# Kernel tuning notes

Hardware: AMD Instinct MI355X
Metric: run time of the kernel (lower is better)

## Reference

```python
import jax, jax.numpy as jnp
import numpy as np

EMBED_DIM = 768
D_K = 64
B, S = 4, 4096


def setup_inputs() -> dict:
    key = jax.random.key(0)
    ks = jax.random.split(key, 7)
    scale = 1.0 / np.sqrt(EMBED_DIM)
    return {
        "x": jax.random.normal(ks[0], (B, S, EMBED_DIM), dtype=jnp.float32),
        "Wq": jax.random.normal(ks[1], (EMBED_DIM, D_K), dtype=jnp.float32) * scale,
        "bq": jax.random.normal(ks[2], (D_K,), dtype=jnp.float32) * 0.01,
        "Wk": jax.random.normal(ks[3], (EMBED_DIM, D_K), dtype=jnp.float32) * scale,
        "bk": jax.random.normal(ks[4], (D_K,), dtype=jnp.float32) * 0.01,
        "Wv": jax.random.normal(ks[5], (EMBED_DIM, D_K), dtype=jnp.float32) * scale,
        "bv": jax.random.normal(ks[6], (D_K,), dtype=jnp.float32) * 0.01,
    }


def reference(x, Wq, bq, Wk, bk, Wv, bv):
    # Linear projections: [B, S, E] @ [E, d_k] + bias -> [B, S, d_k]
    q = jnp.einsum("bse,ed->bsd", x, Wq) + bq
    k = jnp.einsum("bse,ed->bsd", x, Wk) + bk
    v = jnp.einsum("bse,ed->bsd", x, Wv) + bv
    # Scaled dot-product attention; scores: [B, S, S]
    scores = jnp.einsum("bqd,bkd->bqk", q, k) / jnp.sqrt(jnp.asarray(D_K, x.dtype))
    attn = jax.nn.softmax(scores, axis=-1)
    return jnp.einsum("bqk,bkd->bqd", attn, v)
```

## Files before the change

kernel.cpp:

```cpp
#include <hip/hip_runtime.h>

typedef _Float16 f16;
typedef f16 f16x2 __attribute__((ext_vector_type(2)));
typedef f16 f16x4 __attribute__((ext_vector_type(4)));
typedef f16 f16x8 __attribute__((ext_vector_type(8)));
typedef float f32x4 __attribute__((ext_vector_type(4)));

#define MFMA32(A, B, C) __builtin_amdgcn_mfma_f32_16x16x32_f16(A, B, C, 0, 0, 0)
#define MFMA16(A, B, C) __builtin_amdgcn_mfma_f32_16x16x16f16(A, B, C, 0, 0, 0)

#define QSCALE (0.125f * 1.44269504088896340736f)
#define MSHIFT 10.0f

__device__ __forceinline__ f16x2 pkrtz(float a, float b) {
  return __builtin_bit_cast(f16x2, __builtin_amdgcn_cvt_pkrtz(a, b));
}
__device__ __forceinline__ void nts(f16* p, f16x8 v) {
  __builtin_nontemporal_store(v, (f16x8*)p);
}
__device__ __forceinline__ f16x8 ntl(const f16* p) {
  return __builtin_nontemporal_load((const f16x8*)p);
}

__global__ __launch_bounds__(256) void wtrans_kernel(
    const float* __restrict__ Wq, const float* __restrict__ Wk,
    const float* __restrict__ Wv, f16* __restrict__ Wt) {
  __shared__ float T[64][65];
  const int t = threadIdx.x;
  const int kt = blockIdx.x;
  const int z = blockIdx.y;
  const float* W = (z == 0) ? Wq : ((z == 1) ? Wk : Wv);

  {
    const int kl = t >> 2, c0 = (t & 3) * 16;
    const float* wp = W + (kt * 64 + kl) * 64 + c0;
    float4 v0 = *(const float4*)wp;
    float4 v1 = *(const float4*)(wp + 4);
    float4 v2 = *(const float4*)(wp + 8);
    float4 v3 = *(const float4*)(wp + 12);
    float* Tr = &T[kl][c0];
    Tr[0] = v0.x; Tr[1] = v0.y; Tr[2] = v0.z; Tr[3] = v0.w;
    Tr[4] = v1.x; Tr[5] = v1.y; Tr[6] = v1.z; Tr[7] = v1.w;
    Tr[8] = v2.x; Tr[9] = v2.y; Tr[10] = v2.z; Tr[11] = v2.w;
    Tr[12] = v3.x; Tr[13] = v3.y; Tr[14] = v3.z; Tr[15] = v3.w;
  }
  __syncthreads();
  {
    const int n = t >> 2, k0 = (t & 3) * 16;
    union { f16x2 h2[8]; f16x8 h8[2]; } u;
#pragma unroll
    for (int i = 0; i < 8; i++)
      u.h2[i] = pkrtz(T[k0 + 2 * i][n], T[k0 + 2 * i + 1][n]);
    f16* dst = Wt + (z * 64 + n) * 768 + kt * 64 + k0;
    *(f16x8*)dst = u.h8[0];
    *(f16x8*)(dst + 8) = u.h8[1];
  }
}

__global__ __launch_bounds__(256, 4) void proj_kernel(
    const float* __restrict__ x, const f16* __restrict__ Wt,
    const float* __restrict__ bq, const float* __restrict__ bk,
    const float* __restrict__ bv, f16* __restrict__ qo, f16* __restrict__ ko,
    f16* __restrict__ vt) {
  __shared__ f16 Xs[32][72];
  __shared__ f16 Ws[192][72];

  const int t = threadIdx.x;
  const int w = t >> 6;
  const int lane = t & 63;
  const int ln = lane & 15;
  const int quad = lane >> 4;
  const int mh = w & 1;
  const int nh = w >> 1;
  const int r0 = blockIdx.x * 32;

  f32x4 acc[6];
#pragma unroll
  for (int i = 0; i < 6; i++) acc[i] = (f32x4){0.f, 0.f, 0.f, 0.f};

  const int xsr = t >> 3, xsc = (t & 7) * 8;
  const int wsr = t >> 2, wsc = (t & 3) * 16;
  const float* xr = x + (r0 + xsr) * 768 + xsc;
  const f16* wr = Wt + wsr * 768 + wsc;

  float4 xa0, xa1;
  f16x8 wf[3][2];
  xa0 = *(const float4*)xr;
  xa1 = *(const float4*)(xr + 4);
#pragma unroll
  for (int p = 0; p < 3; p++) {
    wf[p][0] = *(const f16x8*)(wr + p * 64 * 768);
    wf[p][1] = *(const f16x8*)(wr + p * 64 * 768 + 8);
  }

  for (int kc = 0; kc < 12; kc++) {
    __syncthreads();
    {
      union { f16x2 h2[4]; f16x8 h8; } u;
      u.h2[0] = pkrtz(xa0.x, xa0.y); u.h2[1] = pkrtz(xa0.z, xa0.w);
      u.h2[2] = pkrtz(xa1.x, xa1.y); u.h2[3] = pkrtz(xa1.z, xa1.w);
      *(f16x8*)&Xs[xsr][xsc] = u.h8;
#pragma unroll
      for (int p = 0; p < 3; p++) {
        *(f16x8*)&Ws[p * 64 + wsr][wsc] = wf[p][0];
        *(f16x8*)&Ws[p * 64 + wsr][wsc + 8] = wf[p][1];
      }
    }
    if (kc + 1 < 12) {
      const float* xp = xr + (kc + 1) * 64;
      xa0 = *(const float4*)xp;
      xa1 = *(const float4*)(xp + 4);
      const f16* wp = wr + (kc + 1) * 64;
#pragma unroll
      for (int p = 0; p < 3; p++) {
        wf[p][0] = *(const f16x8*)(wp + p * 64 * 768);
        wf[p][1] = *(const f16x8*)(wp + p * 64 * 768 + 8);
      }
    }
    __syncthreads();

    f16x8 a0 = *(const f16x8*)&Xs[mh * 16 + ln][quad * 8];
    f16x8 a1 = *(const f16x8*)&Xs[mh * 16 + ln][32 + quad * 8];
#pragma unroll
    for (int nt = 0; nt < 6; nt++) {
      f16x8 b0 = *(const f16x8*)&Ws[nh * 96 + nt * 16 + ln][quad * 8];
      f16x8 b1 = *(const f16x8*)&Ws[nh * 96 + nt * 16 + ln][32 + quad * 8];
      acc[nt] = MFMA32(a0, b0, acc[nt]);
      acc[nt] = MFMA32(a1, b1, acc[nt]);
    }
  }

  const int rowg = r0 + mh * 16 + quad * 4;
  if (nh == 0) {
#pragma unroll
    for (int nt = 0; nt < 4; nt++) {
      int d = nt * 16 + ln;
      float bb = bq[d];
#pragma unroll
      for (int r = 0; r < 4; r++)
        qo[(rowg + r) * 64 + d] = (f16)((acc[nt][r] + bb) * QSCALE);
    }
#pragma unroll
    for (int nt = 4; nt < 6; nt++) {
      int d = nt * 16 + ln - 64;
      float bb = bk[d];
#pragma unroll
      for (int r = 0; r < 4; r++)
        ko[(rowg + r) * 64 + d] = (f16)(acc[nt][r] + bb);
    }
  } else {
#pragma unroll
    for (int nt = 0; nt < 2; nt++) {
      int d = 32 + nt * 16 + ln;
      float bb = bk[d];
#pragma unroll
      for (int r = 0; r < 4; r++)
        ko[(rowg + r) * 64 + d] = (f16)(acc[nt][r] + bb);
    }
    const int bidx = rowg >> 12;
    const int sb = rowg & 4095;
#pragma unroll
    for (int nt = 2; nt < 6; nt++) {
      int dv = nt * 16 + ln - 32;
      float bb = bv[dv];
      f16x4 hv;
#pragma unroll
      for (int r = 0; r < 4; r++) hv[r] = (f16)(acc[nt][r] + bb);
      *(f16x4*)&vt[((bidx * 64 + dv) << 12) + sb] = hv;
    }
  }
}

__global__ __launch_bounds__(512, 4) void attn_kernel(
    const f16* __restrict__ qo, const f16* __restrict__ ko,
    const f16* __restrict__ vt, f16* __restrict__ po, float* __restrict__ pl) {
  constexpr int CS = 8, NK = 4096 / CS;
  __shared__ f16 Ksh[64][76];
  __shared__ f16 Vsh[64][76];

  const int t = threadIdx.x;
  const int w = t >> 6;
  const int lane = t & 63;
  const int ln = lane & 15;
  const int quad = lane >> 4;
  const int bid = blockIdx.x;
  const int c = bid & 7;
  const int qb = bid >> 3;
  const int b = qb >> 4;

  f16x8 bq0[2], bq1[2];
#pragma unroll
  for (int h = 0; h < 2; h++) {
    const int qoff = (qb * 256 + w * 32 + h * 16 + ln) * 64 + quad * 8;
    bq0[h] = *(const f16x8*)(qo + qoff);
    bq1[h] = *(const f16x8*)(qo + qoff + 32);
  }

  f32x4 o[2][4];
#pragma unroll
  for (int h = 0; h < 2; h++)
#pragma unroll
    for (int i = 0; i < 4; i++) o[h][i] = (f32x4){0.f, 0.f, 0.f, 0.f};
  float l_s[2] = {0.f, 0.f};

  const int rr = t >> 3;
  const int cc = (t & 7) * 8;
  const f16* kbase = ko + (b * 4096 + c * NK) * 64;
  const f16* vbase = vt + b * 64 * 4096 + c * NK;

  f16x8 kreg = *(const f16x8*)(kbase + rr * 64 + cc);
  f16x8 vreg = *(const f16x8*)(vbase + rr * 4096 + cc);

  for (int kt = 0; kt < NK / 64; kt++) {
    __syncthreads();
    *(f16x8*)&Ksh[rr][cc] = kreg;
    *(f16x8*)&Vsh[rr][cc] = vreg;
    __syncthreads();

    if (kt + 1 < NK / 64) {
      const int ks1 = (kt + 1) * 64;
      kreg = *(const f16x8*)(kbase + (ks1 + rr) * 64 + cc);
      vreg = *(const f16x8*)(vbase + rr * 4096 + ks1 + cc);
    }

    f16x8 ka[4], kb[4];
#pragma unroll
    for (int nt = 0; nt < 4; nt++) {
      ka[nt] = *(const f16x8*)&Ksh[nt * 16 + ln][quad * 8];
      kb[nt] = *(const f16x8*)&Ksh[nt * 16 + ln][32 + quad * 8];
    }

#pragma unroll
    for (int h = 0; h < 2; h++) {
      f32x4 st[4];
#pragma unroll
      for (int i = 0; i < 4; i++) st[i] = (f32x4){0.f, 0.f, 0.f, 0.f};
#pragma unroll
      for (int nt = 0; nt < 4; nt++) {
        st[nt] = MFMA32(ka[nt], bq0[h], st[nt]);
        st[nt] = MFMA32(kb[nt], bq1[h], st[nt]);
      }

      f16x4 pa[4];
#pragma unroll
      for (int nt = 0; nt < 4; nt++) {
        float p0 = exp2f(st[nt][0] - MSHIFT);
        float p1 = exp2f(st[nt][1] - MSHIFT);
        float p2 = exp2f(st[nt][2] - MSHIFT);
        float p3 = exp2f(st[nt][3] - MSHIFT);
        l_s[h] += (p0 + p1) + (p2 + p3);
        union { f16x2 h2[2]; f16x4 h4; } u;
        u.h2[0] = pkrtz(p0, p1);
        u.h2[1] = pkrtz(p2, p3);
        pa[nt] = u.h4;
      }

#pragma unroll
      for (int nt = 0; nt < 4; nt++)
#pragma unroll
        for (int dt = 0; dt < 4; dt++) {
          f16x4 bv = *(const f16x4*)&Vsh[dt * 16 + ln][nt * 16 + quad * 4];
          o[h][dt] = MFMA16(pa[nt], bv, o[h][dt]);
        }
    }
  }

#pragma unroll
  for (int h = 0; h < 2; h++) {
    const int g = qb * 16 + w * 2 + h;
    union { f16x2 h2[8]; f16x8 h8[2]; } u;
#pragma unroll
    for (int dt = 0; dt < 4; dt++) {
      u.h2[dt * 2] = pkrtz(o[h][dt][0], o[h][dt][1]);
      u.h2[dt * 2 + 1] = pkrtz(o[h][dt][2], o[h][dt][3]);
    }
    f16* p = po + (((size_t)c * 1024 + g) * 64 + lane) * 16;
    nts(p, u.h8[0]);
    nts(p + 8, u.h8[1]);
    float rs = l_s[h];
    rs += __shfl_xor(rs, 16);
    rs += __shfl_xor(rs, 32);
    if (quad == 0) pl[c * 16384 + g * 16 + ln] = rs;
  }
}

__global__ __launch_bounds__(256) void merge_kernel(
    const f16* __restrict__ po, const float* __restrict__ pl,
    float* __restrict__ out) {
  const int t = threadIdx.x;
  const int w = t >> 6;
  const int lane = t & 63;
  const int ln = lane & 15;
  const int quad = lane >> 4;
  const int g = blockIdx.x * 4 + w;

  f32x4 o2[4];
#pragma unroll
  for (int i = 0; i < 4; i++) o2[i] = (f32x4){0.f, 0.f, 0.f, 0.f};
  f32x4 den = (f32x4){0.f, 0.f, 0.f, 0.f};

#pragma unroll
  for (int c = 0; c < 8; c++) {
    f32x4 dv = *(const f32x4*)&pl[c * 16384 + g * 16 + quad * 4];
    den += dv;
    const f16* p = po + (((size_t)c * 1024 + g) * 64 + lane) * 16;
    f16x8 l0 = ntl(p);
    f16x8 l1 = ntl(p + 8);
#pragma unroll
    for (int dt = 0; dt < 2; dt++)
#pragma unroll
      for (int r = 0; r < 4; r++) {
        o2[dt][r] += (float)l0[dt * 4 + r];
        o2[dt + 2][r] += (float)l1[dt * 4 + r];
      }
  }

  const int orow = g * 16 + quad * 4;
#pragma unroll
  for (int r = 0; r < 4; r++) {
    float inv = 1.0f / den[r];
#pragma unroll
    for (int dt = 0; dt < 4; dt++)
      out[(orow + r) * 64 + dt * 16 + ln] = o2[dt][r] * inv;
  }
}

extern "C" void kernel_launch(void* const* d_in, const int* in_sizes, int n_in,
                              void* d_out, int out_size, void* d_ws,
                              size_t ws_size, hipStream_t stream) {
  const float* x = (const float*)d_in[0];
  const float* Wq = (const float*)d_in[1];
  const float* bq = (const float*)d_in[2];
  const float* Wk = (const float*)d_in[3];
  const float* bk = (const float*)d_in[4];
  const float* Wv = (const float*)d_in[5];
  const float* bv = (const float*)d_in[6];
  float* out = (float*)d_out;

  char* ws = (char*)d_ws;
  f16* Wt = (f16*)ws;
  f16* qo = (f16*)(ws + 294912);
  f16* ko = (f16*)(ws + 294912 + 2097152);
  f16* vt = (f16*)(ws + 294912 + 2 * 2097152);
  const size_t base = 6586368;

  f16* po = (f16*)(ws + base);
  float* pl = (float*)(ws + base + (size_t)8 * 16384 * 64 * 2);

  wtrans_kernel<<<dim3(12, 3), dim3(256), 0, stream>>>(Wq, Wk, Wv, Wt);
  proj_kernel<<<dim3(512), dim3(256), 0, stream>>>(x, Wt, bq, bk, bv, qo, ko, vt);
  attn_kernel<<<dim3(512), dim3(512), 0, stream>>>(qo, ko, vt, po, pl);
  merge_kernel<<<dim3(256), dim3(256), 0, stream>>>(po, pl, out);
}
```

Baseline: 144.8 us.

## Switch attention to 32x32x16 MFMA tiles with 32-row query fragments per wave

The attention kernel now uses 32x32x16 f16 MFMA for both QK^T and PV. Each wave owns 32 query rows, and the fixed -MSHIFT offset is folded into the accumulator initialisation. This is meant to cut the instruction count and LDS fragment reads per FLOP compared with the 16x16 tiles. The partial-output layout and the merge kernel change to match the 32x32 accumulator layout, and the merge kernel shares reciprocal denominators through LDS. The change adds register pressure from the f32x16 accumulators and may introduce LDS bank conflicts from the new access pattern.

```diff
diff --git a/kernel.cpp b/kernel.cpp
--- a/kernel.cpp
+++ b/kernel.cpp
@@ -5,9 +5,10 @@
 typedef f16 f16x4 __attribute__((ext_vector_type(4)));
 typedef f16 f16x8 __attribute__((ext_vector_type(8)));
 typedef float f32x4 __attribute__((ext_vector_type(4)));
+typedef float f32x16 __attribute__((ext_vector_type(16)));
 
 #define MFMA32(A, B, C) __builtin_amdgcn_mfma_f32_16x16x32_f16(A, B, C, 0, 0, 0)
-#define MFMA16(A, B, C) __builtin_amdgcn_mfma_f32_16x16x16f16(A, B, C, 0, 0, 0)
+#define MFMAKK(A, B, C) __builtin_amdgcn_mfma_f32_32x32x16_f16(A, B, C, 0, 0, 0)
 
 #define QSCALE (0.125f * 1.44269504088896340736f)
 #define MSHIFT 10.0f
@@ -174,34 +175,33 @@
 __global__ __launch_bounds__(512, 4) void attn_kernel(
     const f16* __restrict__ qo, const f16* __restrict__ ko,
     const f16* __restrict__ vt, f16* __restrict__ po, float* __restrict__ pl) {
-  constexpr int CS = 8, NK = 4096 / CS;
+  constexpr int NK = 512;
   __shared__ f16 Ksh[64][76];
   __shared__ f16 Vsh[64][76];
 
   const int t = threadIdx.x;
   const int w = t >> 6;
   const int lane = t & 63;
-  const int ln = lane & 15;
-  const int quad = lane >> 4;
+  const int l32 = lane & 31;
+  const int hh = lane >> 5;
   const int bid = blockIdx.x;
   const int c = bid & 7;
   const int qb = bid >> 3;
   const int b = qb >> 4;
-
-  f16x8 bq0[2], bq1[2];
-#pragma unroll
-  for (int h = 0; h < 2; h++) {
-    const int qoff = (qb * 256 + w * 32 + h * 16 + ln) * 64 + quad * 8;
-    bq0[h] = *(const f16x8*)(qo + qoff);
-    bq1[h] = *(const f16x8*)(qo + qoff + 32);
-  }
-
-  f32x4 o[2][4];
-#pragma unroll
-  for (int h = 0; h < 2; h++)
-#pragma unroll
-    for (int i = 0; i < 4; i++) o[h][i] = (f32x4){0.f, 0.f, 0.f, 0.f};
-  float l_s[2] = {0.f, 0.f};
+  const int g = qb * 8 + w;
+
+  f16x8 qf[4];
+  {
+    const f16* qp = qo + (size_t)(qb * 256 + w * 32 + l32) * 64 + hh * 8;
+#pragma unroll
+    for (int dblk = 0; dblk < 4; dblk++)
+      qf[dblk] = *(const f16x8*)(qp + dblk * 16);
+  }
+
+  f32x16 o0, o1;
+#pragma unroll
+  for (int r = 0; r < 16; r++) { o0[r] = 0.f; o1[r] = 0.f; }
+  float l_s = 0.f;
 
   const int rr = t >> 3;
   const int cc = (t & 7) * 8;
@@ -223,105 +223,101 @@
       vreg = *(const f16x8*)(vbase + rr * 4096 + ks1 + cc);
     }
 
-    f16x8 ka[4], kb[4];
-#pragma unroll
-    for (int nt = 0; nt < 4; nt++) {
-      ka[nt] = *(const f16x8*)&Ksh[nt * 16 + ln][quad * 8];
-      kb[nt] = *(const f16x8*)&Ksh[nt * 16 + ln][32 + quad * 8];
-    }
-
-#pragma unroll
-    for (int h = 0; h < 2; h++) {
-      f32x4 st[4];
-#pragma unroll
-      for (int i = 0; i < 4; i++) st[i] = (f32x4){0.f, 0.f, 0.f, 0.f};
-#pragma unroll
-      for (int nt = 0; nt < 4; nt++) {
-        st[nt] = MFMA32(ka[nt], bq0[h], st[nt]);
-        st[nt] = MFMA32(kb[nt], bq1[h], st[nt]);
-      }
-
-      f16x4 pa[4];
-#pragma unroll
-      for (int nt = 0; nt < 4; nt++) {
-        float p0 = exp2f(st[nt][0] - MSHIFT);
-        float p1 = exp2f(st[nt][1] - MSHIFT);
-        float p2 = exp2f(st[nt][2] - MSHIFT);
-        float p3 = exp2f(st[nt][3] - MSHIFT);
-        l_s[h] += (p0 + p1) + (p2 + p3);
-        union { f16x2 h2[2]; f16x4 h4; } u;
-        u.h2[0] = pkrtz(p0, p1);
-        u.h2[1] = pkrtz(p2, p3);
-        pa[nt] = u.h4;
-      }
-
-#pragma unroll
-      for (int nt = 0; nt < 4; nt++)
-#pragma unroll
-        for (int dt = 0; dt < 4; dt++) {
-          f16x4 bv = *(const f16x4*)&Vsh[dt * 16 + ln][nt * 16 + quad * 4];
-          o[h][dt] = MFMA16(pa[nt], bv, o[h][dt]);
-        }
-    }
-  }
-
-#pragma unroll
-  for (int h = 0; h < 2; h++) {
-    const int g = qb * 16 + w * 2 + h;
-    union { f16x2 h2[8]; f16x8 h8[2]; } u;
-#pragma unroll
-    for (int dt = 0; dt < 4; dt++) {
-      u.h2[dt * 2] = pkrtz(o[h][dt][0], o[h][dt][1]);
-      u.h2[dt * 2 + 1] = pkrtz(o[h][dt][2], o[h][dt][3]);
-    }
-    f16* p = po + (((size_t)c * 1024 + g) * 64 + lane) * 16;
-    nts(p, u.h8[0]);
-    nts(p + 8, u.h8[1]);
-    float rs = l_s[h];
-    rs += __shfl_xor(rs, 16);
-    rs += __shfl_xor(rs, 32);
-    if (quad == 0) pl[c * 16384 + g * 16 + ln] = rs;
-  }
+#pragma unroll 1
+    for (int kblk = 0; kblk < 2; kblk++) {
+      f32x16 st;
+#pragma unroll
+      for (int r = 0; r < 16; r++) st[r] = -MSHIFT;
+#pragma unroll
+      for (int dblk = 0; dblk < 4; dblk++) {
+        union { f16x4 q4[2]; f16x8 h; } ka;
+        const f16* kp = &Ksh[kblk * 32 + l32][dblk * 16 + hh * 8];
+        ka.q4[0] = *(const f16x4*)(kp);
+        ka.q4[1] = *(const f16x4*)(kp + 4);
+        st = MFMAKK(ka.h, qf[dblk], st);
+      }
+#pragma unroll
+      for (int r = 0; r < 16; r++) {
+        st[r] = exp2f(st[r]);
+        l_s += st[r];
+      }
+      union { f16x2 h2[8]; f16x8 h8[2]; } pu;
+#pragma unroll
+      for (int j = 0; j < 8; j++) pu.h2[j] = pkrtz(st[2 * j], st[2 * j + 1]);
+
+#pragma unroll
+      for (int nt = 0; nt < 2; nt++) {
+        const int kc = kblk * 32 + nt * 16 + 4 * hh;
+        union { f16x4 q4[2]; f16x8 h; } vb0, vb1;
+        vb0.q4[0] = *(const f16x4*)&Vsh[l32][kc];
+        vb0.q4[1] = *(const f16x4*)&Vsh[l32][kc + 8];
+        vb1.q4[0] = *(const f16x4*)&Vsh[32 + l32][kc];
+        vb1.q4[1] = *(const f16x4*)&Vsh[32 + l32][kc + 8];
+        o0 = MFMAKK(pu.h8[nt], vb0.h, o0);
+        o1 = MFMAKK(pu.h8[nt], vb1.h, o1);
+      }
+    }
+  }
+
+  union { f16x2 h2[8]; f16x8 h8[2]; } ua, ub;
+#pragma unroll
+  for (int j = 0; j < 8; j++) {
+    ua.h2[j] = pkrtz(o0[2 * j], o0[2 * j + 1]);
+    ub.h2[j] = pkrtz(o1[2 * j], o1[2 * j + 1]);
+  }
+  f16* p = po + ((size_t)(c * 512 + g) * 64 + lane) * 32;
+  nts(p, ua.h8[0]);
+  nts(p + 8, ua.h8[1]);
+  nts(p + 16, ub.h8[0]);
+  nts(p + 24, ub.h8[1]);
+  float rs = l_s + __shfl_xor(l_s, 32);
+  if (hh == 0) pl[c * 16384 + g * 32 + l32] = rs;
 }
 
 __global__ __launch_bounds__(256) void merge_kernel(
     const f16* __restrict__ po, const float* __restrict__ pl,
     float* __restrict__ out) {
+  __shared__ float inv_sh[4][32];
   const int t = threadIdx.x;
   const int w = t >> 6;
   const int lane = t & 63;
-  const int ln = lane & 15;
-  const int quad = lane >> 4;
+  const int l32 = lane & 31;
+  const int hh = lane >> 5;
   const int g = blockIdx.x * 4 + w;
 
-  f32x4 o2[4];
-#pragma unroll
-  for (int i = 0; i < 4; i++) o2[i] = (f32x4){0.f, 0.f, 0.f, 0.f};
-  f32x4 den = (f32x4){0.f, 0.f, 0.f, 0.f};
-
+  if (hh == 0) {
+    float den = 0.f;
+#pragma unroll
+    for (int c = 0; c < 8; c++) den += pl[c * 16384 + g * 32 + l32];
+    inv_sh[w][l32] = 1.0f / den;
+  }
+
+  float o2a[16], o2b[16];
+#pragma unroll
+  for (int r = 0; r < 16; r++) { o2a[r] = 0.f; o2b[r] = 0.f; }
 #pragma unroll
   for (int c = 0; c < 8; c++) {
-    f32x4 dv = *(const f32x4*)&pl[c * 16384 + g * 16 + quad * 4];
-    den += dv;
-    const f16* p = po + (((size_t)c * 1024 + g) * 64 + lane) * 16;
+    const f16* p = po + ((size_t)(c * 512 + g) * 64 + lane) * 32;
     f16x8 l0 = ntl(p);
     f16x8 l1 = ntl(p + 8);
-#pragma unroll
-    for (int dt = 0; dt < 2; dt++)
-#pragma unroll
-      for (int r = 0; r < 4; r++) {
-        o2[dt][r] += (float)l0[dt * 4 + r];
-        o2[dt + 2][r] += (float)l1[dt * 4 + r];
-      }
-  }
-
-  const int orow = g * 16 + quad * 4;
-#pragma unroll
-  for (int r = 0; r < 4; r++) {
-    float inv = 1.0f / den[r];
-#pragma unroll
-    for (int dt = 0; dt < 4; dt++)
-      out[(orow + r) * 64 + dt * 16 + ln] = o2[dt][r] * inv;
+    f16x8 l2 = ntl(p + 16);
+    f16x8 l3 = ntl(p + 24);
+#pragma unroll
+    for (int r = 0; r < 8; r++) {
+      o2a[r] += (float)l0[r];
+      o2a[r + 8] += (float)l1[r];
+      o2b[r] += (float)l2[r];
+      o2b[r + 8] += (float)l3[r];
+    }
+  }
+  __syncthreads();
+#pragma unroll
+  for (int r = 0; r < 16; r++) {
+    const int q = (r & 3) + 8 * (r >> 2) + 4 * hh;
+    const float inv = inv_sh[w][q];
+    float* orow = out + (size_t)(g * 32 + q) * 64 + l32;
+    orow[0] = o2a[r] * inv;
+    orow[32] = o2b[r] * inv;
   }
 }
 
@@ -345,10 +341,10 @@
   const size_t base = 6586368;
 
   f16* po = (f16*)(ws + base);
-  float* pl = (float*)(ws + base + (size_t)8 * 16384 * 64 * 2);
+  float* pl = (float*)(ws + base + (size_t)8 * 512 * 64 * 32 * 2);
 
   wtrans_kernel<<<dim3(12, 3), dim3(256), 0, stream>>>(Wq, Wk, Wv, Wt);
   proj_kernel<<<dim3(512), dim3(256), 0, stream>>>(x, Wt, bq, bk, bv, qo, ko, vt);
   attn_kernel<<<dim3(512), dim3(512), 0, stream>>>(qo, ko, vt, po, pl);
-  merge_kernel<<<dim3(256), dim3(256), 0, stream>>>(po, pl, out);
-}
+  merge_kernel<<<dim3(128), dim3(256), 0, stream>>>(po, pl, out);
+}
```

New measurement: 147.7 us. +2.0%, slower.
